# Performance work log

Measured on AMD Instinct MI355X. Metric: run time of the kernel, lower is better.

## Reference

```python
import jax, jax.numpy as jnp
import numpy as np

B, CIN, D, H, W = 2, 64, 64, 64, 64
NUM_CLASSES = 5
STRIDE = 2
NMAX = 32
TOPK = 13
TAL_ALPHA, TAL_BETA = 1.0, 6.0
EPS = 1e-9


def setup_inputs() -> dict:
    key = jax.random.key(0)
    ks = jax.random.split(key, 6)
    features = jax.random.normal(ks[0], (B, CIN, D, H, W), jnp.float32)
    cls_w = jax.random.normal(ks[1], (NUM_CLASSES, CIN, 3, 3, 3), jnp.float32) * 0.02
    cls_b = jnp.zeros((NUM_CLASSES,), jnp.float32)
    off_w = jax.random.normal(ks[2], (3, CIN, 3, 3, 3), jnp.float32) * 0.01
    off_b = jnp.zeros((3,), jnp.float32)
    coords = jax.random.uniform(ks[3], (B, NMAX, 3), jnp.float32, 4.0, float(D * STRIDE) - 4.0)
    cls = jax.random.randint(ks[4], (B, NMAX, 1), 0, NUM_CLASSES).astype(jnp.float32)
    sigma = jax.random.uniform(ks[5], (B, NMAX, 1), jnp.float32, 2.0, 8.0)
    pad = (jnp.arange(NMAX) >= 24)[None, :, None]  # last 8 GT slots are padding
    cls = jnp.where(pad, -100.0, cls)
    labels = jnp.concatenate([coords, cls, sigma], axis=-1)  # B N 5 : x,y,z,class,sigma
    return {"features": features, "cls_w": cls_w, "cls_b": cls_b,
            "off_w": off_w, "off_b": off_b, "labels": labels}


def conv3d(x, w, b):
    y = jax.lax.conv_general_dilated(x, w, (1, 1, 1), 'SAME',
                                     dimension_numbers=('NCDHW', 'OIDHW', 'NCDHW'))
    return y + b[None, :, None, None, None]


def make_anchors():
    g = jnp.stack(jnp.meshgrid(jnp.arange(D), jnp.arange(H), jnp.arange(W), indexing='ij'))
    return (g.astype(jnp.float32) + 0.5) * STRIDE  # (3, D, H, W)


def flatten_bchw(x):
    # B C D H W -> B (D H W) C
    Bsz, C = x.shape[0], x.shape[1]
    return x.transpose(0, 2, 3, 4, 1).reshape(Bsz, -1, C)


def tal_assign(pred_logits, pred_centers, true_labels, true_centers, true_sigmas, valid):
    # pred_logits (B,L,C); pred_centers (B,L,3); true_* (B,N,...); valid (B,N) bool
    Bsz, L, C = pred_logits.shape
    N = true_labels.shape[1]
    d2 = jnp.sum((true_centers[:, :, None, :] - pred_centers[:, None, :, :]) ** 2, -1)  # B N L
    ious = jnp.exp(-d2 / (2.0 * true_sigmas[:, :, None] ** 2))  # keypoint IoU, B N L
    probs = jax.nn.sigmoid(pred_logits).transpose(0, 2, 1)  # B C L
    cls_scores = jnp.take_along_axis(probs, true_labels[:, :, None], axis=1)  # B N L
    align = (cls_scores ** TAL_ALPHA) * (ious ** TAL_BETA)  # alignment metric
    topv, topi = jax.lax.top_k(align, TOPK)
    is_topk = jnp.zeros_like(align).at[
        jnp.arange(Bsz)[:, None, None], jnp.arange(N)[None, :, None], topi
    ].set(jnp.where(topv > EPS, 1.0, 0.0))
    mask_pos = is_topk * valid[:, :, None].astype(align.dtype)  # B N L
    pos_sum = mask_pos.sum(axis=1)  # B L
    # resolve anchors matched to multiple GTs: keep GT with max IoU
    is_max_iou = jax.nn.one_hot(jnp.argmax(ious, axis=1), N, axis=1, dtype=align.dtype)
    mask_pos = jnp.where(pos_sum[:, None, :] > 1, is_max_iou, mask_pos)
    pos_sum = mask_pos.sum(axis=1)
    fg = pos_sum > 0  # B L
    assigned_gt = jnp.argmax(mask_pos, axis=1)  # B L
    assigned_labels = jnp.take_along_axis(true_labels, assigned_gt, axis=1)
    assigned_labels = jnp.where(fg, assigned_labels, C)  # bg_index = C
    assigned_centers = jnp.take_along_axis(true_centers, assigned_gt[:, :, None], axis=1)  # B L 3
    assigned_sigmas = jnp.take_along_axis(true_sigmas, assigned_gt, axis=1)  # B L
    align = align * mask_pos
    max_align = align.max(axis=2, keepdims=True)  # B N 1
    max_iou = (ious * mask_pos).max(axis=2, keepdims=True)
    score = (align * max_iou / (max_align + EPS)).max(axis=1)  # B L
    assigned_scores = jax.nn.one_hot(assigned_labels, C + 1)[..., :C] * score[..., None]  # B L C
    return assigned_labels, assigned_centers, assigned_scores, assigned_sigmas


def detection_loss(logits, offsets, anchors, labels):
    pred_logits = flatten_bchw(logits)               # B L C
    pred_centers = flatten_bchw(anchors + offsets)   # B L 3
    anchor_pts = flatten_bchw(anchors)
    C = pred_logits.shape[-1]
    true_centers = labels[..., :3]
    true_labels_f = labels[..., 3]
    true_sigmas = labels[..., 4]
    valid = true_labels_f != -100.0
    true_labels = jnp.where(valid, true_labels_f, 0.0).astype(jnp.int32)
    assigned = tal_assign(jax.lax.stop_gradient(pred_logits),
                          jax.lax.stop_gradient(pred_centers),
                          true_labels, true_centers, true_sigmas, valid)
    assigned_labels, assigned_centers, assigned_scores, assigned_sigmas = jax.lax.stop_gradient(assigned)
    one_hot_label = jax.nn.one_hot(assigned_labels, C + 1)[..., :C]
    # varifocal loss (alpha=0.75, gamma=2)
    p = jax.nn.sigmoid(pred_logits)
    weight = 0.75 * (p ** 2.0) * (1.0 - one_hot_label) + assigned_scores * one_hot_label
    bce = assigned_scores * jax.nn.softplus(-pred_logits) + (1.0 - assigned_scores) * jax.nn.softplus(pred_logits)
    cls_loss = jnp.sum(weight * bce)
    d = jnp.sum((pred_centers - assigned_centers) ** 2, -1)  # B L
    w = assigned_scores.sum(-1)
    iou = jnp.exp(-d / (2.0 * assigned_sigmas ** 2))
    mask_positive = assigned_labels != C
    reg_loss = jnp.sum(jnp.where(mask_positive, (1.0 - iou) * w, 0.0))
    return (cls_loss + reg_loss) / assigned_scores.sum()


def reference(features, cls_w, cls_b, off_w, off_b, labels):
    logits = conv3d(features, cls_w, cls_b)    # B C D H W
    offsets = conv3d(features, off_w, off_b)   # B 3 D H W
    anchors = jnp.broadcast_to(make_anchors()[None], (features.shape[0], 3, D, H, W))
    loss = detection_loss(logits, offsets, anchors, labels)
    return loss
```

## Files before the change

### kernel.cpp

```cpp
#include <hip/hip_runtime.h>
#include <math.h>

#define NB 2
#define CIN 64
#define DD_ 64
#define HH_ 64
#define WW_ 64
#define NCLS 5
#define LL (DD_*HH_*WW_)
#define NMAXG 32
#define TOPKK 13
#define NSLAB 4

typedef __attribute__((ext_vector_type(8)))  short short8b;
typedef __attribute__((ext_vector_type(16))) float floatx16;

__device__ __forceinline__ float softplusf_(float z){
  return fmaxf(z, 0.f) + log1pf(expf(-fabsf(z)));
}
__device__ __forceinline__ float sigmoidf_(float z){
  return 1.f/(1.f + expf(-z));
}
__device__ __forceinline__ unsigned tobf_u_(float f){
  unsigned u = __float_as_uint(f);
  return (u + 0x7fffu + ((u>>16)&1u)) >> 16;
}
__device__ __forceinline__ short tobf_(float f){
  return (short)tobf_u_(f);
}

__global__ __launch_bounds__(256) void transpose_kernel(
    const float* __restrict__ feat, short* __restrict__ featT,
    const float* __restrict__ cls_w, const float* __restrict__ off_w,
    short* __restrict__ wA, float* __restrict__ bgz)
{
  const int t = threadIdx.x;
  const int w = t & 63;
  const int hh = t >> 6;
  const int d = blockIdx.x;
  const int h = blockIdx.y*4 + hh;
  const int b = blockIdx.z;
  const float* src = feat + (size_t)b*CIN*LL + (size_t)d*4096 + (size_t)h*64 + w;
  const size_t sp = (size_t)d*4096 + (size_t)h*64 + w;
  #pragma unroll
  for (int cc=0; cc<4; ++cc){
    float f[16];
    #pragma unroll
    for (int j=0;j<16;++j) f[j] = src[(size_t)(cc*16+j)*LL];
    uint4 p0, p1;
    p0.x = (tobf_u_(f[1])<<16)|tobf_u_(f[0]);  p0.y = (tobf_u_(f[3])<<16)|tobf_u_(f[2]);
    p0.z = (tobf_u_(f[5])<<16)|tobf_u_(f[4]);  p0.w = (tobf_u_(f[7])<<16)|tobf_u_(f[6]);
    p1.x = (tobf_u_(f[9])<<16)|tobf_u_(f[8]);  p1.y = (tobf_u_(f[11])<<16)|tobf_u_(f[10]);
    p1.z = (tobf_u_(f[13])<<16)|tobf_u_(f[12]);p1.w = (tobf_u_(f[15])<<16)|tobf_u_(f[14]);
    *(uint4*)(featT + (((size_t)(b*4+cc)*2 + 0)*LL + sp)*8) = p0;
    *(uint4*)(featT + (((size_t)(b*4+cc)*2 + 1)*LL + sp)*8) = p1;
  }
  if (blockIdx.z == 0 && blockIdx.y == 0 && blockIdx.x < 54){
    if (blockIdx.x == 0 && t < 2) bgz[t] = 0.f;
    int idx = blockIdx.x*256 + t;
    int slice = idx >> 6; int lane = idx & 63;
    int cc = slice & 3; int r = slice >> 2;
    int kw = r % 3; int r2 = r / 3;
    int kh = r2 % 3; int rr = r2 / 3;
    int m = lane & 31, khalf = lane >> 5;
    int outch = m & 7;
    int kd = rr - (m >> 3);
    short8b out;
    #pragma unroll
    for (int i=0;i<8;++i){
      int c = cc*16 + khalf*8 + i;
      float wv = 0.f;
      if (kd >= 0 && kd <= 2){
        if (outch < NCLS) wv = cls_w[(outch*CIN + c)*27 + kd*9 + kh*3 + kw];
        else              wv = off_w[((outch-NCLS)*CIN + c)*27 + kd*9 + kh*3 + kw];
      }
      out[i] = tobf_(wv);
    }
    *(short8b*)(wA + (size_t)idx*8) = out;
  }
}

__global__ __launch_bounds__(256, 2) void conv_mfma_kernel(
    const short* __restrict__ featT,
    const short* __restrict__ wA,
    const float* __restrict__ cls_b, const float* __restrict__ off_b,
    float* __restrict__ logits_ws,
    float* __restrict__ centers_ws,
    float* __restrict__ bg_sum,
    unsigned* __restrict__ moff_u)
{
  __shared__ short xs[36*132*8];
  __shared__ float bsum[4];

  const int tid = threadIdx.x;
  const int lane = tid & 63, hl = tid >> 6;
  const int col = lane & 31, khalf = lane >> 5;
  const int h0 = blockIdx.x*4, d0 = blockIdx.y*4, b = blockIdx.z;
  const bool edge = (d0==0) || (d0==DD_-4) || (h0==0) || (h0==HH_-4);

  for (int idx = tid; idx < 144; idx += 256){
    int row = idx >> 2, q = idx & 3;
    *(uint4*)(xs + (row*132 + (q>>1)*66 + (q&1)*65)*8) = make_uint4(0,0,0,0);
  }
  if (edge){
    #pragma unroll 1
    for (int row=0; row<36; ++row){
      int d_ = d0-1+row/6, h_ = h0-1+row-6*(row/6);
      if ((unsigned)d_ < 64u && (unsigned)h_ < 64u) continue;
      if (tid < 128){
        int kh2 = tid >> 6, wp = (tid & 63) + 1;
        *(uint4*)(xs + (row*132 + kh2*66 + wp)*8) = make_uint4(0,0,0,0);
      }
    }
  }

  int soff[18]; int sdst[18]; unsigned svalid = 0;
  #pragma unroll
  for (int it=0; it<18; ++it){
    int strip = it*4 + hl;
    int row = strip >> 1, kh2 = strip & 1;
    int rd = row/6;
    int d_ = d0 - 1 + rd, h_ = h0 - 1 + row - 6*rd;
    bool v = !edge || ((unsigned)d_ < 64u && (unsigned)h_ < 64u);
    if (v) svalid |= (1u<<it);
    int dc = v ? d_ : 0, hc = v ? h_ : 0;
    soff[it] = (kh2*LL + dc*4096 + hc*64 + lane)*8;
    sdst[it] = (row*132 + kh2*66 + 1)*8;
  }

  floatx16 accA = (floatx16)(0.f);
  floatx16 accB = (floatx16)(0.f);

  const short8b* wAv = (const short8b*)wA;
  const short* bp0 = xs + hl*1056 + khalf*528 + col*8;

#define STAGE(ccv) { \
  const short* plane = featT + (size_t)(b*4+(ccv))*2*(size_t)LL*8; \
  _Pragma("unroll") \
  for (int it=0; it<18; ++it){ \
    if (svalid & (1u<<it)){ \
      __builtin_amdgcn_global_load_lds( \
        (const __attribute__((address_space(1))) void*)(plane + soff[it]), \
        (__attribute__((address_space(3))) void*)(xs + sdst[it]), 16, 0, 0); \
    } \
  } }

#define LOADA(dst, ccv, rrv) { \
  _Pragma("unroll") \
  for (int q=0;q<9;++q) dst[q] = wAv[(size_t)((((rrv)*9+q)*4+(ccv)))*64 + lane]; }

#define COMPR(areg, rrv) \
  if ((unsigned)(d0-1+(rrv)) < 64u){ \
    const short* bp = bp0 + (rrv)*6336; \
    _Pragma("unroll") \
    for (int kh=0;kh<3;++kh){ \
      if ((unsigned)(h0+hl-1+kh) < 64u){ \
        _Pragma("unroll") \
        for (int kw=0;kw<3;++kw){ \
          short8b a = areg[kh*3+kw]; \
          short8b b0 = *(const short8b*)(bp + kh*1056 + kw*8); \
          accA = __builtin_amdgcn_mfma_f32_32x32x16_bf16(a, b0, accA, 0,0,0); \
          short8b b1 = *(const short8b*)(bp + kh*1056 + kw*8 + 256); \
          accB = __builtin_amdgcn_mfma_f32_32x32x16_bf16(a, b1, accB, 0,0,0); \
        } } } }

  short8b aP[9], aQ[9];
  LOADA(aP, 0, 0);

  #pragma unroll 1
  for (int cc=0; cc<4; ++cc){
    if (cc) __syncthreads();
    STAGE(cc);
    __syncthreads();
    LOADA(aQ, cc, 1);             COMPR(aP, 0);
    LOADA(aP, cc, 2);             COMPR(aQ, 1);
    LOADA(aQ, cc, 3);             COMPR(aP, 2);
    LOADA(aP, cc, 4);             COMPR(aQ, 3);
    LOADA(aQ, cc, 5);             COMPR(aP, 4);
    { int nc = (cc+1)&3; LOADA(aP, nc, 0); }  COMPR(aQ, 5);
  }

  float bg = 0.f, om = 0.f;
  const int h = h0 + hl;
  #pragma unroll
  for (int wh=0; wh<2; ++wh){
    const int w = wh*32 + col;
    #pragma unroll
    for (int dq=0; dq<4; ++dq){
      int d = d0 + dq;
      size_t l = (size_t)d*4096 + (size_t)h*64 + w;
      float v0 = wh ? accB[dq*4+0] : accA[dq*4+0];
      float v1 = wh ? accB[dq*4+1] : accA[dq*4+1];
      float v2 = wh ? accB[dq*4+2] : accA[dq*4+2];
      float v3 = wh ? accB[dq*4+3] : accA[dq*4+3];
      if (khalf == 0){
        float z0 = v0 + cls_b[0]; logits_ws[(size_t)(b*NCLS+0)*LL + l] = z0;
        float z1 = v1 + cls_b[1]; logits_ws[(size_t)(b*NCLS+1)*LL + l] = z1;
        float z2 = v2 + cls_b[2]; logits_ws[(size_t)(b*NCLS+2)*LL + l] = z2;
        float z3 = v3 + cls_b[3]; logits_ws[(size_t)(b*NCLS+3)*LL + l] = z3;
        float p;
        p = sigmoidf_(z0); bg += 0.75f*p*p*softplusf_(z0);
        p = sigmoidf_(z1); bg += 0.75f*p*p*softplusf_(z1);
        p = sigmoidf_(z2); bg += 0.75f*p*p*softplusf_(z2);
        p = sigmoidf_(z3); bg += 0.75f*p*p*softplusf_(z3);
      } else {
        float z4 = v0 + cls_b[4]; logits_ws[(size_t)(b*NCLS+4)*LL + l] = z4;
        float p = sigmoidf_(z4); bg += 0.75f*p*p*softplusf_(z4);
        float o0 = v1 + off_b[0];
        float o1 = v2 + off_b[1];
        float o2 = v3 + off_b[2];
        om = fmaxf(om, fmaxf(fabsf(o0), fmaxf(fabsf(o1), fabsf(o2))));
        float4 ctr;
        ctr.x = ((float)d+0.5f)*2.f + o0;
        ctr.y = ((float)h+0.5f)*2.f + o1;
        ctr.z = ((float)w+0.5f)*2.f + o2;
        ctr.w = 0.f;
        *(float4*)(centers_ws + ((size_t)b*LL + l)*4) = ctr;
      }
    }
  }
  #pragma unroll
  for (int off=32;off;off>>=1){
    bg += __shfl_down(bg, off);
    om = fmaxf(om, __shfl_xor(om, off));
  }
  if (lane == 0){
    bsum[hl] = bg;
    atomicMax(moff_u, __float_as_uint(om));
  }
  __syncthreads();
  if (tid == 0)
    atomicAdd(bg_sum, bsum[0]+bsum[1]+bsum[2]+bsum[3]);
}

__global__ __launch_bounds__(256) void topk_box_kernel(
    const float* __restrict__ logits_ws, const float* __restrict__ centers_ws,
    const float* __restrict__ labels,
    const unsigned* __restrict__ moff_u,
    float* __restrict__ pv, int* __restrict__ pi)
{
  const int bn = blockIdx.x;
  const int slab = blockIdx.y;
  const int b = bn >> 5, n = bn & 31;
  const int tid = threadIdx.x;

  const float* lb = labels + (b*NMAXG + n)*5;
  const float tx = lb[0], ty = lb[1], tz = lb[2];
  const float cf = lb[3];
  const float sg = lb[4];
  const int lab = (cf == -100.f) ? 0 : (int)cf;
  const float m6 = -3.f/(sg*sg);
  const float moff = __uint_as_float(*moff_u);
  const float R = 2.6336f*sg + moff + 0.05f;

  int i0d = (int)ceilf((tx - R - 1.f)*0.5f); if (i0d < 0) i0d = 0;
  int i1d = (int)floorf((tx + R - 1.f)*0.5f); if (i1d > 63) i1d = 63;
  int i0h = (int)ceilf((ty - R - 1.f)*0.5f); if (i0h < 0) i0h = 0;
  int i1h = (int)floorf((ty + R - 1.f)*0.5f); if (i1h > 63) i1h = 63;
  int i0w = (int)ceilf((tz - R - 1.f)*0.5f); if (i0w < 0) i0w = 0;
  int i1w = (int)floorf((tz + R - 1.f)*0.5f); if (i1w > 63) i1w = 63;
  int nd = i1d-i0d+1, nh = i1h-i0h+1, nw = i1w-i0w+1;
  int total = (nd>0 && nh>0 && nw>0) ? nd*nh*nw : 0;
  int lo = (total*slab)/NSLAB, hi = (total*(slab+1))/NSLAB;

  const float* lg = logits_ws + (size_t)(b*NCLS + lab)*LL;
  const float* cb = centers_ws + (size_t)b*LL*4;

  float v[13]; int ix[13];
  #pragma unroll
  for (int j=0;j<13;++j){ v[j]=-1.f; ix[j]=0x7fffffff; }

  for (int idx = lo + tid; idx < hi; idx += 256){
    int r = idx;
    int wi = r % nw; r /= nw;
    int hi2 = r % nh; int di = r / nh;
    int l = (i0d+di)*4096 + (i0h+hi2)*64 + (i0w+wi);
    float4 c4 = *(const float4*)(cb + (size_t)l*4);
    float dx = c4.x-tx, dy = c4.y-ty, dz = c4.z-tz;
    float e = m6*(dx*dx + dy*dy + dz*dz);
    if (e < -20.8f) continue;
    float a = sigmoidf_(lg[l]) * expf(e);
    if (a > v[12]){
      float cv = a; int ci = l;
      #pragma unroll
      for (int j=0;j<13;++j){
        bool take = (cv > v[j]) || (cv == v[j] && ci < ix[j]);
        float nv = take ? cv : v[j];  float ov = take ? v[j] : cv;
        int   ni = take ? ci : ix[j]; int   oi = take ? ix[j] : ci;
        v[j]=nv; ix[j]=ni; cv=ov; ci=oi;
      }
    }
  }

  const int lane = tid & 63, wvi = tid >> 6;
  float mv = -2.f; int mi = 0x7fffffff;
  #pragma unroll 1
  for (int k=0;k<13;++k){
    float bv = v[0]; int bi = ix[0]; int bl = lane;
    #pragma unroll
    for (int off=32; off; off>>=1){
      float ov2 = __shfl_xor(bv, off);
      int oi = __shfl_xor(bi, off);
      int ol = __shfl_xor(bl, off);
      if (ov2 > bv || (ov2 == bv && oi < bi)){ bv=ov2; bi=oi; bl=ol; }
    }
    if (lane == k){ mv = bv; mi = bi; }
    if (lane == bl){
      #pragma unroll
      for (int j=0;j<12;++j){ v[j]=v[j+1]; ix[j]=ix[j+1]; }
      v[12] = -2.f; ix[12] = 0x7fffffff;
    }
  }
  __shared__ float sv2[4*13]; __shared__ int si2[4*13];
  if (lane < 13){ sv2[wvi*13+lane] = mv; si2[wvi*13+lane] = mi; }
  __syncthreads();
  if (wvi == 0){
    float v2 = -2.f; int i2 = 0x7fffffff;
    if (lane < 52){ v2 = sv2[lane]; i2 = si2[lane]; }
    #pragma unroll 1
    for (int k=0;k<13;++k){
      float bv = v2; int bi = i2; int bl = lane;
      #pragma unroll
      for (int off=32; off; off>>=1){
        float ov2 = __shfl_xor(bv, off);
        int oi = __shfl_xor(bi, off);
        int ol = __shfl_xor(bl, off);
        if (ov2 > bv || (ov2 == bv && oi < bi)){ bv=ov2; bi=oi; bl=ol; }
      }
      if (lane == 0){
        pv[(bn*NSLAB+slab)*TOPKK + k] = bv;
        pi[(bn*NSLAB+slab)*TOPKK + k] = bi;
      }
      if (lane == bl) v2 = -2.f;
    }
  }
}

__global__ __launch_bounds__(64) void topk_merge_kernel(
    const float* __restrict__ pv, const int* __restrict__ pi,
    float* __restrict__ tv, int* __restrict__ ti)
{
  const int bn = blockIdx.x;
  const int t = threadIdx.x;
  const int NC = NSLAB*TOPKK;
  float v = -2.f; int ix = 0x7fffffff;
  if (t < NC){ v = pv[bn*NC + t]; ix = pi[bn*NC + t]; }
  #pragma unroll 1
  for (int k=0;k<13;++k){
    float bv = v; int bi = ix; int bl = t;
    #pragma unroll
    for (int off=32; off; off>>=1){
      float ov = __shfl_xor(bv, off);
      int oi = __shfl_xor(bi, off);
      int ol = __shfl_xor(bl, off);
      if (ov > bv || (ov == bv && oi < bi)){ bv=ov; bi=oi; bl=ol; }
    }
    if (t==0){ tv[bn*TOPKK+k]=bv; ti[bn*TOPKK+k]=bi; }
    if (t==bl) v = -2.f;
  }
}

__global__ __launch_bounds__(1024) void finalize_kernel(
    const float* __restrict__ logits_ws, const float* __restrict__ centers_ws,
    const float* __restrict__ labels,
    const float* __restrict__ tv, const int* __restrict__ ti,
    const float* __restrict__ bg_sum, float* __restrict__ out)
{
  const int tid = threadIdx.x;
  __shared__ float gx[64], gy[64], gz[64], gs[64];
  __shared__ int glab[64], gvalid[64];
  __shared__ int hkey[2048], hcnt[2048], hmin[2048];
  __shared__ unsigned maxA[64], maxI[64];
  __shared__ float accD, accC;
  if (tid==0){ accD=0.f; accC=0.f; }
  for (int i=tid;i<2048;i+=1024){ hkey[i]=-1; hcnt[i]=0; hmin[i]=0x7fffffff; }
  if (tid<64){
    const float* lb = labels + tid*5;
    gx[tid]=lb[0]; gy[tid]=lb[1]; gz[tid]=lb[2];
    float cf = lb[3]; gs[tid]=lb[4];
    int val = (cf != -100.f);
    gvalid[tid]=val; glab[tid]= val ? (int)cf : 0;
    maxA[tid]=0u; maxI[tid]=0u;
  }
  __syncthreads();

  const int e = tid;
  bool ok = false; int l = -1; int n = 0; int b = 0;
  if (e < 2*416){
    b = (e >= 416) ? 1 : 0;
    int eb = e - 416*b;
    n = eb/13; int k = eb - 13*n;
    float v = tv[(b*NMAXG+n)*TOPKK + k];
    l = ti[(b*NMAXG+n)*TOPKK + k];
    ok = gvalid[b*32+n] && (v > 1e-9f);
  }
  int slot = -1;
  if (ok){
    unsigned h = (((unsigned)l * 2654435761u) >> 20) & 1023u;
    for (;;){
      int prev = atomicCAS(&hkey[b*1024 + h], -1, l);
      if (prev == -1 || prev == l){ slot = b*1024 + (int)h; break; }
      h = (h+1) & 1023u;
    }
    atomicAdd(&hcnt[slot], 1);
    atomicMin(&hmin[slot], e);
  }
  __syncthreads();

  bool first = ok && (hmin[slot] == e);
  float a=0.f, iou=0.f; int nstar=0;
  if (first){
    float px = centers_ws[((size_t)b*LL + l)*4 + 0];
    float py = centers_ws[((size_t)b*LL + l)*4 + 1];
    float pz = centers_ws[((size_t)b*LL + l)*4 + 2];
    if (hcnt[slot] == 1){
      nstar = n;
    } else {
      float best = -1.f; int bidx = 0;
      #pragma unroll 1
      for (int nn=0;nn<32;++nn){
        float dx=gx[b*32+nn]-px, dy=gy[b*32+nn]-py, dz=gz[b*32+nn]-pz;
        float d2 = dx*dx+dy*dy+dz*dz;
        float io = expf(-d2/(2.f*gs[b*32+nn]*gs[b*32+nn]));
        if (io > best){ best=io; bidx=nn; }
      }
      nstar = bidx;
    }
    int gi = b*32 + nstar;
    float dx=gx[gi]-px, dy=gy[gi]-py, dz=gz[gi]-pz;
    float d2 = dx*dx+dy*dy+dz*dz;
    float sgv = gs[gi];
    iou = expf(-d2/(2.f*sgv*sgv));
    float z = logits_ws[(size_t)(b*NCLS + glab[gi])*LL + l];
    a = sigmoidf_(z) * expf(-3.f*d2/(sgv*sgv));
    atomicMax(&maxA[gi], __float_as_uint(a));
    atomicMax(&maxI[gi], __float_as_uint(iou));
  }
  __syncthreads();

  if (first){
    int gi = b*32 + nstar;
    float mA = __uint_as_float(maxA[gi]);
    float mI = __uint_as_float(maxI[gi]);
    float score = a*mI/(mA + 1e-9f);
    float z = logits_ws[(size_t)(b*NCLS + glab[gi])*LL + l];
    float p = sigmoidf_(z);
    float t2 = log1pf(expf(-fabsf(z)));
    float spz = fmaxf(z,0.f) + t2;
    float spm = fmaxf(-z,0.f) + t2;
    float corr = score*(score*spm + (1.f-score)*spz) - 0.75f*p*p*spz;
    float reg  = (1.f - iou)*score;
    atomicAdd(&accD, score);
    atomicAdd(&accC, corr + reg);
  }
  __syncthreads();
  if (tid==0) out[0] = (bg_sum[0] + accC) / accD;
}

extern "C" void kernel_launch(void* const* d_in, const int* in_sizes, int n_in,
                              void* d_out, int out_size, void* d_ws, size_t ws_size,
                              hipStream_t stream) {
  const float* feat  = (const float*)d_in[0];
  const float* cls_w = (const float*)d_in[1];
  const float* cls_b = (const float*)d_in[2];
  const float* off_w = (const float*)d_in[3];
  const float* off_b = (const float*)d_in[4];
  const float* labels= (const float*)d_in[5];
  float* out = (float*)d_out;

  float* logits_ws  = (float*)d_ws;
  float* centers_ws = logits_ws + (size_t)NB*NCLS*LL;
  float* tv = centers_ws + (size_t)NB*LL*4;
  int*   ti = (int*)(tv + 64*TOPKK);
  float* pv = (float*)(ti + 64*TOPKK);
  int*   pi = (int*)(pv + 64*NSLAB*TOPKK);
  float* bg = (float*)(pi + 64*NSLAB*TOPKK);
  short* wA = (short*)(bg + 16);
  short* featT = wA + 216*64*8;

  transpose_kernel<<<dim3(64,16,2), 256, 0, stream>>>(
      feat, featT, cls_w, off_w, wA, bg);
  conv_mfma_kernel<<<dim3(16,16,2), 256, 0, stream>>>(
      featT, wA, cls_b, off_b, logits_ws, centers_ws, bg, (unsigned*)(bg+1));
  topk_box_kernel<<<dim3(64,NSLAB), 256, 0, stream>>>(
      logits_ws, centers_ws, labels, (const unsigned*)(bg+1), pv, pi);
  topk_merge_kernel<<<64, 64, 0, stream>>>(pv, pi, tv, ti);
  finalize_kernel<<<1, 1024, 0, stream>>>(
      logits_ws, centers_ws, labels, tv, ti, bg, out);
}
```

Before: 167.1 us.

## Fuse feature bf16 transpose into conv staging and merge top-k into finalize

Drops the separate transpose kernel that wrote a bf16 channel-packed copy of the features. The conv kernel now reads fp32 features directly, converts them to bf16 in registers and writes them to LDS, replacing the async global_load_lds path. The top-k merge kernel is also folded into the single-block finalize kernel, which reduces its results into shared memory. This removes a full write and re-read of the transposed feature tensor and two launches. In exchange, conv staging becomes synchronous strided fp32 loads, each thread reading 8 channel planes per strip, which may expose load latency and lower overlap with the MFMA work.

After: 194.8 us. 1.17x slower.

```diff
diff --git a/kernel.cpp b/kernel.cpp
--- a/kernel.cpp
+++ b/kernel.cpp
@@ -29,59 +29,36 @@
   return (short)tobf_u_(f);
 }
 
-__global__ __launch_bounds__(256) void transpose_kernel(
-    const float* __restrict__ feat, short* __restrict__ featT,
+__global__ __launch_bounds__(256) void wtrans_kernel(
     const float* __restrict__ cls_w, const float* __restrict__ off_w,
     short* __restrict__ wA, float* __restrict__ bgz)
 {
-  const int t = threadIdx.x;
-  const int w = t & 63;
-  const int hh = t >> 6;
-  const int d = blockIdx.x;
-  const int h = blockIdx.y*4 + hh;
-  const int b = blockIdx.z;
-  const float* src = feat + (size_t)b*CIN*LL + (size_t)d*4096 + (size_t)h*64 + w;
-  const size_t sp = (size_t)d*4096 + (size_t)h*64 + w;
+  if (blockIdx.x == 0 && threadIdx.x < 2) bgz[threadIdx.x] = 0.f;
+  int idx = blockIdx.x*256 + threadIdx.x;
+  if (idx >= 216*64) return;
+  int slice = idx >> 6; int lane = idx & 63;
+  int cc = slice & 3; int r = slice >> 2;
+  int kw = r % 3; int r2 = r / 3;
+  int kh = r2 % 3; int rr = r2 / 3;
+  int m = lane & 31, khalf = lane >> 5;
+  int outch = m & 7;
+  int kd = rr - (m >> 3);
+  short8b out;
   #pragma unroll
-  for (int cc=0; cc<4; ++cc){
-    float f[16];
-    #pragma unroll
-    for (int j=0;j<16;++j) f[j] = src[(size_t)(cc*16+j)*LL];
-    uint4 p0, p1;
-    p0.x = (tobf_u_(f[1])<<16)|tobf_u_(f[0]);  p0.y = (tobf_u_(f[3])<<16)|tobf_u_(f[2]);
-    p0.z = (tobf_u_(f[5])<<16)|tobf_u_(f[4]);  p0.w = (tobf_u_(f[7])<<16)|tobf_u_(f[6]);
-    p1.x = (tobf_u_(f[9])<<16)|tobf_u_(f[8]);  p1.y = (tobf_u_(f[11])<<16)|tobf_u_(f[10]);
-    p1.z = (tobf_u_(f[13])<<16)|tobf_u_(f[12]);p1.w = (tobf_u_(f[15])<<16)|tobf_u_(f[14]);
-    *(uint4*)(featT + (((size_t)(b*4+cc)*2 + 0)*LL + sp)*8) = p0;
-    *(uint4*)(featT + (((size_t)(b*4+cc)*2 + 1)*LL + sp)*8) = p1;
-  }
-  if (blockIdx.z == 0 && blockIdx.y == 0 && blockIdx.x < 54){
-    if (blockIdx.x == 0 && t < 2) bgz[t] = 0.f;
-    int idx = blockIdx.x*256 + t;
-    int slice = idx >> 6; int lane = idx & 63;
-    int cc = slice & 3; int r = slice >> 2;
-    int kw = r % 3; int r2 = r / 3;
-    int kh = r2 % 3; int rr = r2 / 3;
-    int m = lane & 31, khalf = lane >> 5;
-    int outch = m & 7;
-    int kd = rr - (m >> 3);
-    short8b out;
-    #pragma unroll
-    for (int i=0;i<8;++i){
-      int c = cc*16 + khalf*8 + i;
-      float wv = 0.f;
-      if (kd >= 0 && kd <= 2){
-        if (outch < NCLS) wv = cls_w[(outch*CIN + c)*27 + kd*9 + kh*3 + kw];
-        else              wv = off_w[((outch-NCLS)*CIN + c)*27 + kd*9 + kh*3 + kw];
-      }
-      out[i] = tobf_(wv);
-    }
-    *(short8b*)(wA + (size_t)idx*8) = out;
-  }
+  for (int i=0;i<8;++i){
+    int c = cc*16 + khalf*8 + i;
+    float wv = 0.f;
+    if (kd >= 0 && kd <= 2){
+      if (outch < NCLS) wv = cls_w[(outch*CIN + c)*27 + kd*9 + kh*3 + kw];
+      else              wv = off_w[((outch-NCLS)*CIN + c)*27 + kd*9 + kh*3 + kw];
+    }
+    out[i] = tobf_(wv);
+  }
+  *(short8b*)(wA + (size_t)idx*8) = out;
 }
 
 __global__ __launch_bounds__(256, 2) void conv_mfma_kernel(
-    const short* __restrict__ featT,
+    const float* __restrict__ feat,
     const short* __restrict__ wA,
     const float* __restrict__ cls_b, const float* __restrict__ off_b,
     float* __restrict__ logits_ws,
@@ -101,17 +78,6 @@
   for (int idx = tid; idx < 144; idx += 256){
     int row = idx >> 2, q = idx & 3;
     *(uint4*)(xs + (row*132 + (q>>1)*66 + (q&1)*65)*8) = make_uint4(0,0,0,0);
-  }
-  if (edge){
-    #pragma unroll 1
-    for (int row=0; row<36; ++row){
-      int d_ = d0-1+row/6, h_ = h0-1+row-6*(row/6);
-      if ((unsigned)d_ < 64u && (unsigned)h_ < 64u) continue;
-      if (tid < 128){
-        int kh2 = tid >> 6, wp = (tid & 63) + 1;
-        *(uint4*)(xs + (row*132 + kh2*66 + wp)*8) = make_uint4(0,0,0,0);
-      }
-    }
   }
 
   int soff[18]; int sdst[18]; unsigned svalid = 0;
@@ -124,8 +90,8 @@
     bool v = !edge || ((unsigned)d_ < 64u && (unsigned)h_ < 64u);
     if (v) svalid |= (1u<<it);
     int dc = v ? d_ : 0, hc = v ? h_ : 0;
-    soff[it] = (kh2*LL + dc*4096 + hc*64 + lane)*8;
-    sdst[it] = (row*132 + kh2*66 + 1)*8;
+    soff[it] = kh2*8*LL + dc*4096 + hc*64 + lane;
+    sdst[it] = (row*132 + kh2*66 + 1 + lane)*8;
   }
 
   floatx16 accA = (floatx16)(0.f);
@@ -133,16 +99,21 @@
 
   const short8b* wAv = (const short8b*)wA;
   const short* bp0 = xs + hl*1056 + khalf*528 + col*8;
+  const float* fbase = feat + (size_t)b*CIN*LL;
 
 #define STAGE(ccv) { \
-  const short* plane = featT + (size_t)(b*4+(ccv))*2*(size_t)LL*8; \
+  const float* fb_ = fbase + (size_t)(ccv)*16*LL; \
   _Pragma("unroll") \
   for (int it=0; it<18; ++it){ \
+    uint4 pk = make_uint4(0u,0u,0u,0u); \
     if (svalid & (1u<<it)){ \
-      __builtin_amdgcn_global_load_lds( \
-        (const __attribute__((address_space(1))) void*)(plane + soff[it]), \
-        (__attribute__((address_space(3))) void*)(xs + sdst[it]), 16, 0, 0); \
+      const float* sp_ = fb_ + soff[it]; \
+      pk.x = (tobf_u_(sp_[(size_t)1*LL])<<16)|tobf_u_(sp_[0]); \
+      pk.y = (tobf_u_(sp_[(size_t)3*LL])<<16)|tobf_u_(sp_[(size_t)2*LL]); \
+      pk.z = (tobf_u_(sp_[(size_t)5*LL])<<16)|tobf_u_(sp_[(size_t)4*LL]); \
+      pk.w = (tobf_u_(sp_[(size_t)7*LL])<<16)|tobf_u_(sp_[(size_t)6*LL]); \
     } \
+    *(uint4*)(xs + sdst[it]) = pk; \
   } }
 
 #define LOADA(dst, ccv, rrv) { \
@@ -336,34 +307,10 @@
   }
 }
 
-__global__ __launch_bounds__(64) void topk_merge_kernel(
-    const float* __restrict__ pv, const int* __restrict__ pi,
-    float* __restrict__ tv, int* __restrict__ ti)
-{
-  const int bn = blockIdx.x;
-  const int t = threadIdx.x;
-  const int NC = NSLAB*TOPKK;
-  float v = -2.f; int ix = 0x7fffffff;
-  if (t < NC){ v = pv[bn*NC + t]; ix = pi[bn*NC + t]; }
-  #pragma unroll 1
-  for (int k=0;k<13;++k){
-    float bv = v; int bi = ix; int bl = t;
-    #pragma unroll
-    for (int off=32; off; off>>=1){
-      float ov = __shfl_xor(bv, off);
-      int oi = __shfl_xor(bi, off);
-      int ol = __shfl_xor(bl, off);
-      if (ov > bv || (ov == bv && oi < bi)){ bv=ov; bi=oi; bl=ol; }
-    }
-    if (t==0){ tv[bn*TOPKK+k]=bv; ti[bn*TOPKK+k]=bi; }
-    if (t==bl) v = -2.f;
-  }
-}
-
 __global__ __launch_bounds__(1024) void finalize_kernel(
     const float* __restrict__ logits_ws, const float* __restrict__ centers_ws,
     const float* __restrict__ labels,
-    const float* __restrict__ tv, const int* __restrict__ ti,
+    const float* __restrict__ pv, const int* __restrict__ pi,
     const float* __restrict__ bg_sum, float* __restrict__ out)
 {
   const int tid = threadIdx.x;
@@ -371,6 +318,7 @@
   __shared__ int glab[64], gvalid[64];
   __shared__ int hkey[2048], hcnt[2048], hmin[2048];
   __shared__ unsigned maxA[64], maxI[64];
+  __shared__ float tvs[64*TOPKK]; __shared__ int tis[64*TOPKK];
   __shared__ float accD, accC;
   if (tid==0){ accD=0.f; accC=0.f; }
   for (int i=tid;i<2048;i+=1024){ hkey[i]=-1; hcnt[i]=0; hmin[i]=0x7fffffff; }
@@ -382,6 +330,30 @@
     gvalid[tid]=val; glab[tid]= val ? (int)cf : 0;
     maxA[tid]=0u; maxI[tid]=0u;
   }
+
+  {
+    const int lane = tid & 63, wvi = tid >> 6;
+    const int NC = NSLAB*TOPKK;
+    #pragma unroll 1
+    for (int q=0; q<4; ++q){
+      int bn = wvi*4 + q;
+      float v = -2.f; int ix = 0x7fffffff;
+      if (lane < NC){ v = pv[bn*NC + lane]; ix = pi[bn*NC + lane]; }
+      #pragma unroll 1
+      for (int k=0;k<13;++k){
+        float bv = v; int bi = ix; int bl = lane;
+        #pragma unroll
+        for (int off=32; off; off>>=1){
+          float ov = __shfl_xor(bv, off);
+          int oi = __shfl_xor(bi, off);
+          int ol = __shfl_xor(bl, off);
+          if (ov > bv || (ov == bv && oi < bi)){ bv=ov; bi=oi; bl=ol; }
+        }
+        if (lane==0){ tvs[bn*TOPKK+k]=bv; tis[bn*TOPKK+k]=bi; }
+        if (lane==bl) v = -2.f;
+      }
+    }
+  }
   __syncthreads();
 
   const int e = tid;
@@ -390,8 +362,8 @@
     b = (e >= 416) ? 1 : 0;
     int eb = e - 416*b;
     n = eb/13; int k = eb - 13*n;
-    float v = tv[(b*NMAXG+n)*TOPKK + k];
-    l = ti[(b*NMAXG+n)*TOPKK + k];
+    float v = tvs[(b*NMAXG+n)*TOPKK + k];
+    l = tis[(b*NMAXG+n)*TOPKK + k];
     ok = gvalid[b*32+n] && (v > 1e-9f);
   }
   int slot = -1;
@@ -470,21 +442,16 @@
 
   float* logits_ws  = (float*)d_ws;
   float* centers_ws = logits_ws + (size_t)NB*NCLS*LL;
-  float* tv = centers_ws + (size_t)NB*LL*4;
-  int*   ti = (int*)(tv + 64*TOPKK);
-  float* pv = (float*)(ti + 64*TOPKK);
+  float* pv = centers_ws + (size_t)NB*LL*4;
   int*   pi = (int*)(pv + 64*NSLAB*TOPKK);
   float* bg = (float*)(pi + 64*NSLAB*TOPKK);
   short* wA = (short*)(bg + 16);
-  short* featT = wA + 216*64*8;
-
-  transpose_kernel<<<dim3(64,16,2), 256, 0, stream>>>(
-      feat, featT, cls_w, off_w, wA, bg);
+
+  wtrans_kernel<<<54, 256, 0, stream>>>(cls_w, off_w, wA, bg);
   conv_mfma_kernel<<<dim3(16,16,2), 256, 0, stream>>>(
-      featT, wA, cls_b, off_b, logits_ws, centers_ws, bg, (unsigned*)(bg+1));
+      feat, wA, cls_b, off_b, logits_ws, centers_ws, bg, (unsigned*)(bg+1));
   topk_box_kernel<<<dim3(64,NSLAB), 256, 0, stream>>>(
       logits_ws, centers_ws, labels, (const unsigned*)(bg+1), pv, pi);
-  topk_merge_kernel<<<64, 64, 0, stream>>>(pv, pi, tv, ti);
   finalize_kernel<<<1, 1024, 0, stream>>>(
-      logits_ws, centers_ws, labels, tv, ti, bg, out);
-}
+      logits_ws, centers_ws, labels, pv, pi, bg, out);
+}
```

## Switch conv to FP8 MFMA with double-buffered LDS staging

Applied to the files above, without the earlier changes.

Features and weights are now quantized to FP8 (e4m3) instead of bf16, and the conv uses the fp8 32x32x16 MFMA. This halves the featT workspace traffic and the LDS footprint per stage. That frees room to double-buffer the LDS tile, so the next channel chunk is staged while the current one computes. The cost is lower numeric precision in the conv outputs, which feed top-k assignment and the loss and could change results.

Result: no change. 164.0 us (-1.9%).

```diff
diff --git a/kernel.cpp b/kernel.cpp
--- a/kernel.cpp
+++ b/kernel.cpp
@@ -11,8 +11,8 @@
 #define NMAXG 32
 #define TOPKK 13
 #define NSLAB 4
-
-typedef __attribute__((ext_vector_type(8)))  short short8b;
+#define BUFSZ 38016
+
 typedef __attribute__((ext_vector_type(16))) float floatx16;
 
 __device__ __forceinline__ float softplusf_(float z){
@@ -21,18 +21,27 @@
 __device__ __forceinline__ float sigmoidf_(float z){
   return 1.f/(1.f + expf(-z));
 }
-__device__ __forceinline__ unsigned tobf_u_(float f){
-  unsigned u = __float_as_uint(f);
-  return (u + 0x7fffu + ((u>>16)&1u)) >> 16;
-}
-__device__ __forceinline__ short tobf_(float f){
-  return (short)tobf_u_(f);
+__device__ __forceinline__ unsigned tofp8_(float x){
+  unsigned u = __float_as_uint(x);
+  unsigned sign = (u >> 24) & 0x80u;
+  unsigned a = u & 0x7FFFFFFFu;
+  if (a >= 0x43E00000u) return sign | 0x7Eu;
+  if (a < 0x3C800000u){
+    float fa = __uint_as_float(a);
+    int m = (int)rintf(fa * 512.f);
+    return sign | (unsigned)m;
+  }
+  unsigned bb = a + 0x7FFFFu + ((a >> 20) & 1u);
+  unsigned e8 = ((bb >> 23) & 0xFFu) - 120u;
+  unsigned m8 = (bb >> 20) & 7u;
+  if (e8 > 15u || (e8 == 15u && m8 > 6u)) return sign | 0x7Eu;
+  return sign | (e8 << 3) | m8;
 }
 
 __global__ __launch_bounds__(256) void transpose_kernel(
-    const float* __restrict__ feat, short* __restrict__ featT,
+    const float* __restrict__ feat, unsigned char* __restrict__ featT,
     const float* __restrict__ cls_w, const float* __restrict__ off_w,
-    short* __restrict__ wA, float* __restrict__ bgz)
+    unsigned char* __restrict__ wA, float* __restrict__ bgz)
 {
   const int t = threadIdx.x;
   const int w = t & 63;
@@ -44,16 +53,15 @@
   const size_t sp = (size_t)d*4096 + (size_t)h*64 + w;
   #pragma unroll
   for (int cc=0; cc<4; ++cc){
-    float f[16];
+    unsigned q[16];
     #pragma unroll
-    for (int j=0;j<16;++j) f[j] = src[(size_t)(cc*16+j)*LL];
-    uint4 p0, p1;
-    p0.x = (tobf_u_(f[1])<<16)|tobf_u_(f[0]);  p0.y = (tobf_u_(f[3])<<16)|tobf_u_(f[2]);
-    p0.z = (tobf_u_(f[5])<<16)|tobf_u_(f[4]);  p0.w = (tobf_u_(f[7])<<16)|tobf_u_(f[6]);
-    p1.x = (tobf_u_(f[9])<<16)|tobf_u_(f[8]);  p1.y = (tobf_u_(f[11])<<16)|tobf_u_(f[10]);
-    p1.z = (tobf_u_(f[13])<<16)|tobf_u_(f[12]);p1.w = (tobf_u_(f[15])<<16)|tobf_u_(f[14]);
-    *(uint4*)(featT + (((size_t)(b*4+cc)*2 + 0)*LL + sp)*8) = p0;
-    *(uint4*)(featT + (((size_t)(b*4+cc)*2 + 1)*LL + sp)*8) = p1;
+    for (int j=0;j<16;++j) q[j] = tofp8_(src[(size_t)(cc*16+j)*LL]);
+    uint4 p;
+    p.x = q[0] | (q[1]<<8) | (q[2]<<16) | (q[3]<<24);
+    p.y = q[4] | (q[5]<<8) | (q[6]<<16) | (q[7]<<24);
+    p.z = q[8] | (q[9]<<8) | (q[10]<<16) | (q[11]<<24);
+    p.w = q[12] | (q[13]<<8) | (q[14]<<16) | (q[15]<<24);
+    *(uint4*)(featT + ((size_t)(b*4+cc)*LL + sp)*16) = p;
   }
   if (blockIdx.z == 0 && blockIdx.y == 0 && blockIdx.x < 54){
     if (blockIdx.x == 0 && t < 2) bgz[t] = 0.f;
@@ -65,7 +73,7 @@
     int m = lane & 31, khalf = lane >> 5;
     int outch = m & 7;
     int kd = rr - (m >> 3);
-    short8b out;
+    unsigned q[8];
     #pragma unroll
     for (int i=0;i<8;++i){
       int c = cc*16 + khalf*8 + i;
@@ -74,23 +82,27 @@
         if (outch < NCLS) wv = cls_w[(outch*CIN + c)*27 + kd*9 + kh*3 + kw];
         else              wv = off_w[((outch-NCLS)*CIN + c)*27 + kd*9 + kh*3 + kw];
       }
-      out[i] = tobf_(wv);
-    }
-    *(short8b*)(wA + (size_t)idx*8) = out;
+      q[i] = tofp8_(wv);
+    }
+    uint2 p;
+    p.x = q[0] | (q[1]<<8) | (q[2]<<16) | (q[3]<<24);
+    p.y = q[4] | (q[5]<<8) | (q[6]<<16) | (q[7]<<24);
+    *(uint2*)(wA + (size_t)idx*8) = p;
   }
 }
 
 __global__ __launch_bounds__(256, 2) void conv_mfma_kernel(
-    const short* __restrict__ featT,
-    const short* __restrict__ wA,
+    const unsigned char* __restrict__ featT,
+    const unsigned char* __restrict__ wA,
     const float* __restrict__ cls_b, const float* __restrict__ off_b,
     float* __restrict__ logits_ws,
     float* __restrict__ centers_ws,
     float* __restrict__ bg_sum,
     unsigned* __restrict__ moff_u)
 {
-  __shared__ short xs[36*132*8];
+  __shared__ uint4 xs4[2*BUFSZ/16];
   __shared__ float bsum[4];
+  unsigned char* xs = (unsigned char*)xs4;
 
   const int tid = threadIdx.x;
   const int lane = tid & 63, hl = tid >> 6;
@@ -99,8 +111,9 @@
   const bool edge = (d0==0) || (d0==DD_-4) || (h0==0) || (h0==HH_-4);
 
   for (int idx = tid; idx < 144; idx += 256){
-    int row = idx >> 2, q = idx & 3;
-    *(uint4*)(xs + (row*132 + (q>>1)*66 + (q&1)*65)*8) = make_uint4(0,0,0,0);
+    int buf = idx / 72; int j = idx - buf*72;
+    int row = j >> 1, slot = j & 1;
+    *(uint4*)(xs + buf*BUFSZ + row*1056 + slot*1040) = make_uint4(0,0,0,0);
   }
   if (edge){
     #pragma unroll 1
@@ -108,76 +121,77 @@
       int d_ = d0-1+row/6, h_ = h0-1+row-6*(row/6);
       if ((unsigned)d_ < 64u && (unsigned)h_ < 64u) continue;
       if (tid < 128){
-        int kh2 = tid >> 6, wp = (tid & 63) + 1;
-        *(uint4*)(xs + (row*132 + kh2*66 + wp)*8) = make_uint4(0,0,0,0);
-      }
-    }
-  }
-
-  int soff[18]; int sdst[18]; unsigned svalid = 0;
+        int buf = tid >> 6, wp = (tid & 63) + 1;
+        *(uint4*)(xs + buf*BUFSZ + row*1056 + wp*16) = make_uint4(0,0,0,0);
+      }
+    }
+  }
+
+  int soff[9]; int sdst[9]; unsigned svalid = 0;
   #pragma unroll
-  for (int it=0; it<18; ++it){
-    int strip = it*4 + hl;
-    int row = strip >> 1, kh2 = strip & 1;
+  for (int it=0; it<9; ++it){
+    int row = it*4 + hl;
     int rd = row/6;
     int d_ = d0 - 1 + rd, h_ = h0 - 1 + row - 6*rd;
     bool v = !edge || ((unsigned)d_ < 64u && (unsigned)h_ < 64u);
     if (v) svalid |= (1u<<it);
     int dc = v ? d_ : 0, hc = v ? h_ : 0;
-    soff[it] = (kh2*LL + dc*4096 + hc*64 + lane)*8;
-    sdst[it] = (row*132 + kh2*66 + 1)*8;
+    soff[it] = (dc*4096 + hc*64 + lane)*16;
+    sdst[it] = row*1056 + 16;
   }
 
   floatx16 accA = (floatx16)(0.f);
   floatx16 accB = (floatx16)(0.f);
 
-  const short8b* wAv = (const short8b*)wA;
-  const short* bp0 = xs + hl*1056 + khalf*528 + col*8;
-
-#define STAGE(ccv) { \
-  const short* plane = featT + (size_t)(b*4+(ccv))*2*(size_t)LL*8; \
+  const long* wAv = (const long*)wA;
+  const int bpoff = hl*1056 + col*16 + khalf*8;
+
+#define STAGE(ccv, bufsel) { \
+  const unsigned char* plane = featT + (size_t)(b*4+(ccv))*LL*16; \
   _Pragma("unroll") \
-  for (int it=0; it<18; ++it){ \
+  for (int it=0; it<9; ++it){ \
     if (svalid & (1u<<it)){ \
       __builtin_amdgcn_global_load_lds( \
         (const __attribute__((address_space(1))) void*)(plane + soff[it]), \
-        (__attribute__((address_space(3))) void*)(xs + sdst[it]), 16, 0, 0); \
+        (__attribute__((address_space(3))) void*)(xs + (bufsel)*BUFSZ + sdst[it]), 16, 0, 0); \
     } \
   } }
 
 #define LOADA(dst, ccv, rrv) { \
   _Pragma("unroll") \
-  for (int q=0;q<9;++q) dst[q] = wAv[(size_t)((((rrv)*9+q)*4+(ccv)))*64 + lane]; }
-
-#define COMPR(areg, rrv) \
+  for (int q=0;q<9;++q) dst[q] = wAv[(size_t)(((rrv)*9+q)*4+(ccv))*64 + lane]; }
+
+#define COMPR(areg, rrv, xb) \
   if ((unsigned)(d0-1+(rrv)) < 64u){ \
-    const short* bp = bp0 + (rrv)*6336; \
+    const unsigned char* bp = (xb) + bpoff + (rrv)*6336; \
     _Pragma("unroll") \
     for (int kh=0;kh<3;++kh){ \
       if ((unsigned)(h0+hl-1+kh) < 64u){ \
         _Pragma("unroll") \
         for (int kw=0;kw<3;++kw){ \
-          short8b a = areg[kh*3+kw]; \
-          short8b b0 = *(const short8b*)(bp + kh*1056 + kw*8); \
-          accA = __builtin_amdgcn_mfma_f32_32x32x16_bf16(a, b0, accA, 0,0,0); \
-          short8b b1 = *(const short8b*)(bp + kh*1056 + kw*8 + 256); \
-          accB = __builtin_amdgcn_mfma_f32_32x32x16_bf16(a, b1, accB, 0,0,0); \
+          long a = areg[kh*3+kw]; \
+          long b0 = *(const long*)(bp + kh*1056 + kw*16); \
+          accA = __builtin_amdgcn_mfma_f32_32x32x16_fp8_fp8(a, b0, accA, 0,0,0); \
+          long b1 = *(const long*)(bp + kh*1056 + kw*16 + 512); \
+          accB = __builtin_amdgcn_mfma_f32_32x32x16_fp8_fp8(a, b1, accB, 0,0,0); \
         } } } }
 
-  short8b aP[9], aQ[9];
+  long aP[9], aQ[9];
   LOADA(aP, 0, 0);
+  STAGE(0, 0);
+  __syncthreads();
 
   #pragma unroll 1
   for (int cc=0; cc<4; ++cc){
-    if (cc) __syncthreads();
-    STAGE(cc);
+    if (cc < 3) STAGE(cc+1, (cc+1)&1);
+    const unsigned char* xb = xs + (cc&1)*BUFSZ;
+    LOADA(aQ, cc, 1);             COMPR(aP, 0, xb);
+    LOADA(aP, cc, 2);             COMPR(aQ, 1, xb);
+    LOADA(aQ, cc, 3);             COMPR(aP, 2, xb);
+    LOADA(aP, cc, 4);             COMPR(aQ, 3, xb);
+    LOADA(aQ, cc, 5);             COMPR(aP, 4, xb);
+    { int nc = (cc+1)&3; LOADA(aP, nc, 0); }  COMPR(aQ, 5, xb);
     __syncthreads();
-    LOADA(aQ, cc, 1);             COMPR(aP, 0);
-    LOADA(aP, cc, 2);             COMPR(aQ, 1);
-    LOADA(aQ, cc, 3);             COMPR(aP, 2);
-    LOADA(aP, cc, 4);             COMPR(aQ, 3);
-    LOADA(aQ, cc, 5);             COMPR(aP, 4);
-    { int nc = (cc+1)&3; LOADA(aP, nc, 0); }  COMPR(aQ, 5);
   }
 
   float bg = 0.f, om = 0.f;
@@ -475,8 +489,8 @@
   float* pv = (float*)(ti + 64*TOPKK);
   int*   pi = (int*)(pv + 64*NSLAB*TOPKK);
   float* bg = (float*)(pi + 64*NSLAB*TOPKK);
-  short* wA = (short*)(bg + 16);
-  short* featT = wA + 216*64*8;
+  unsigned char* wA = (unsigned char*)(bg + 16);
+  unsigned char* featT = wA + 216*64*8;
 
   transpose_kernel<<<dim3(64,16,2), 256, 0, stream>>>(
       feat, featT, cls_w, off_w, wA, bg);
```
